# Kernel optimization log

Hardware: AMD Instinct MI355X
Metric: run time of the kernel (lower is better)

Reference implementation:

```python
import jax, jax.numpy as jnp
import numpy as np

R = 12          # resolution (H = W = G); L = R**3 = 1728
HEADS = 12


def setup_inputs() -> dict:
    key = jax.random.key(0)
    k1, k2, k3 = jax.random.split(key, 3)
    B, L, C = 4, R ** 3, 768
    qkv = jax.random.normal(k1, (3, B, L, C), dtype=jnp.float32)
    lepe_w = jax.random.normal(k2, (C, 1, 3, 3, 3), dtype=jnp.float32) * 0.05
    lepe_b = jax.random.normal(k3, (C,), dtype=jnp.float32) * 0.01
    return {"qkv": qkv, "lepe_w": lepe_w, "lepe_b": lepe_b}


def reference(qkv, lepe_w, lepe_b):
    # qkv: [3, B, L, C]; idx=0 => window == full volume, so attention is dense over L.
    q, k, v = qkv[0], qkv[1], qkv[2]
    B, L, C = q.shape
    hd = C // HEADS
    scale = hd ** -0.5

    # im2cswin with full-volume window preserves token order: [B, L, C] -> [B, H, L, d]
    qh = q.reshape(B, L, HEADS, hd).transpose(0, 2, 1, 3)
    kh = k.reshape(B, L, HEADS, hd).transpose(0, 2, 1, 3)

    # get_lepe: v -> [B, C, R, R, R], depthwise 3x3x3 conv (groups=C)
    v_img = v.transpose(0, 2, 1).reshape(B, C, R, R, R)
    lepe = jax.lax.conv_general_dilated(
        v_img, lepe_w, window_strides=(1, 1, 1), padding="SAME",
        dimension_numbers=("NCDHW", "OIDHW", "NCDHW"), feature_group_count=C,
    ) + lepe_b[None, :, None, None, None]
    lepe = lepe.reshape(B, HEADS, hd, L).transpose(0, 1, 3, 2)   # [B, H, L, d]
    vh = v_img.reshape(B, HEADS, hd, L).transpose(0, 1, 3, 2)    # [B, H, L, d]

    attn = jax.nn.softmax(jnp.einsum("bhqd,bhkd->bhqk", qh * scale, kh), axis=-1)
    out = jnp.einsum("bhqk,bhkd->bhqd", attn, vh) + lepe          # [B, H, L, d]

    # windows2img with full window is an inverse reshape back to [B, L, C]
    return out.transpose(0, 2, 1, 3).reshape(B, L, C)
```

## Files before the change

kernel.cpp:

```cpp
#include <hip/hip_runtime.h>

#define RR 12
#define LL 1728
#define CC 768
#define HEADS 12
#define HD 64
#define BATCH 4

typedef __attribute__((ext_vector_type(8))) short bf8;
typedef __attribute__((ext_vector_type(4))) float f4;

__device__ inline unsigned short f2bf(float x) {
  unsigned int u = __float_as_uint(x);
  return (unsigned short)((u + 0x7FFFu + ((u >> 16) & 1u)) >> 16);
}
__device__ inline unsigned short f2bfr(float x) {
  return (unsigned short)((__float_as_uint(x) + 0x8000u) >> 16);
}

__device__ inline float fast_exp2(float x) {
#if __has_builtin(__builtin_amdgcn_exp2f)
  return __builtin_amdgcn_exp2f(x);
#else
  return exp2f(x);
#endif
}

__device__ inline void gld16(const unsigned short* g, unsigned short* l) {
  __builtin_amdgcn_global_load_lds((const __attribute__((address_space(1))) unsigned int*)g,
                                   (__attribute__((address_space(3))) unsigned int*)l, 16, 0, 0);
}

#define QSCALE 0.1803368801111244f

#define NLEPE 5184
#define NPREP 1296

__global__ __launch_bounds__(256) void combined_kernel(const float* __restrict__ qkv,
                                                       const float* __restrict__ w,
                                                       const float* __restrict__ bias,
                                                       unsigned short* __restrict__ qb,
                                                       unsigned short* __restrict__ kb,
                                                       unsigned short* __restrict__ vT,
                                                       float* __restrict__ out) {
  __shared__ __align__(16) unsigned char smem[27648];
  const int bid = blockIdx.x;
  const int t = threadIdx.x;

  if (bid < NLEPE) {
    const int xg = (bid % 3) * 4;
    const int line = (bid / 3) % 144;
    const int ct = (bid / 432) % 3;
    const int b = bid / 1296;
    const int z = line / RR;
    const int y = line % RR;
    const int c0 = ct * 256;
    const int c = c0 + t;
    float* w_lds = (float*)smem;

    {
      const float* wsrc = w + (size_t)c0 * 27;
#pragma unroll
      for (int i = 0; i < 7; ++i) {
        const int idx = i * 256 + t;
        if (idx < 1728) *(float4*)&w_lds[idx * 4] = *(const float4*)&wsrc[idx * 4];
      }
    }
    __syncthreads();
    float wreg[27];
#pragma unroll
    for (int j = 0; j < 27; ++j) wreg[j] = w_lds[t * 27 + j];

    const float* vb = qkv + ((size_t)(2 * BATCH + b)) * LL * CC + c;
    const float bv = bias[c];
    float acc[4] = {bv, bv, bv, bv};

#pragma unroll
    for (int dz = -1; dz <= 1; ++dz) {
#pragma unroll
      for (int dy = -1; dy <= 1; ++dy) {
        const int zz = z + dz, yy = y + dy;
        const bool lineok = ((unsigned)zz < RR) & ((unsigned)yy < RR);
        const int base = (zz * RR + yy) * RR;
        float v6[6];
#pragma unroll
        for (int p = 0; p < 6; ++p) {
          const int xx = xg - 1 + p;
          const bool ok = lineok & ((unsigned)xx < RR);
          const int lp = ok ? base + xx : 0;
          const float vv = vb[(size_t)lp * CC];
          v6[p] = ok ? vv : 0.f;
        }
        const int jb = ((dz + 1) * 3 + (dy + 1)) * 3;
        const float wL = wreg[jb], wC = wreg[jb + 1], wR = wreg[jb + 2];
#pragma unroll
        for (int i = 0; i < 4; ++i)
          acc[i] += wL * v6[i] + wC * v6[i + 1] + wR * v6[i + 2];
      }
    }
    const size_t obase = ((size_t)b * LL + line * RR + xg) * CC + c;
#pragma unroll
    for (int i = 0; i < 4; ++i) out[obase + (size_t)i * CC] = acc[i];

  } else {
    const int p = bid - NLEPE;
    const int lt = p % 27;
    const int h = (p / 27) % HEADS;
    const int b = p / (27 * HEADS);
    unsigned short* tl = (unsigned short*)smem;

    {
      const int r0 = t >> 4;
      const int c4 = (t & 15) * 4;
#pragma unroll
      for (int pi = 0; pi < 4; ++pi) {
        const int row = lt * 64 + pi * 16 + r0;
        const size_t off = ((size_t)b * LL + row) * CC + h * HD + c4;
        const float4 qv = *(const float4*)(qkv + off);
        ushort4 oq;
        oq.x = f2bf(qv.x * QSCALE); oq.y = f2bf(qv.y * QSCALE);
        oq.z = f2bf(qv.z * QSCALE); oq.w = f2bf(qv.w * QSCALE);
        *(ushort4*)(qb + off) = oq;
        const float4 kv = *(const float4*)(qkv + (size_t)BATCH * LL * CC + off);
        ushort4 ok;
        ok.x = f2bf(kv.x); ok.y = f2bf(kv.y); ok.z = f2bf(kv.z); ok.w = f2bf(kv.w);
        *(ushort4*)(kb + off) = ok;
      }
    }

    const float* vsrc = qkv + ((size_t)(2 * BATCH + b)) * LL * CC;
#pragma unroll
    for (int it = 0; it < 4; ++it) {
      const int idx = it * 256 + t;
      const int lrow = idx >> 4;
      const int c4 = (idx & 15) * 4;
      const float4 vv = *(const float4*)(vsrc + (size_t)(lt * 64 + lrow) * CC + h * HD + c4);
      tl[(c4 + 0) * 65 + lrow] = f2bf(vv.x);
      tl[(c4 + 1) * 65 + lrow] = f2bf(vv.y);
      tl[(c4 + 2) * 65 + lrow] = f2bf(vv.z);
      tl[(c4 + 3) * 65 + lrow] = f2bf(vv.w);
    }
    __syncthreads();
#pragma unroll
    for (int it = 0; it < 4; ++it) {
      const int idx = it * 256 + t;
      const int drow = idx >> 4;
      const int s4 = (idx & 15) * 4;
      const int lb = s4 >> 2;
      ushort4 o;
      o.x = tl[drow * 65 + lb];
      o.y = tl[drow * 65 + 16 + lb];
      o.z = tl[drow * 65 + 32 + lb];
      o.w = tl[drow * 65 + 48 + lb];
      *(ushort4*)(vT + (((size_t)(b * HEADS + h) * HD + drow) * LL) + lt * 64 + s4) = o;
    }
  }
}

__global__ __launch_bounds__(256) void attn_kernel(const unsigned short* __restrict__ qb,
                                                   const unsigned short* __restrict__ kb,
                                                   const unsigned short* __restrict__ vT,
                                                   float* __restrict__ out) {
  __shared__ unsigned short k_lds[2][64 * 64];
  __shared__ unsigned short v_lds[2][64 * 64];
  __shared__ unsigned short p_lds[4][16 * 72];

  const int qt = blockIdx.x;
  const int h = blockIdx.y;
  const int b = blockIdx.z;
  const int t = threadIdx.x;
  const int lane = t & 63;
  const int wave = t >> 6;
  const int m = lane & 15;
  const int quad = lane >> 4;

  bf8 qf[2];
  {
    const size_t qbase = ((size_t)(b * LL + qt * 64 + wave * 16 + m)) * CC + h * HD;
    qf[0] = *(const bf8*)(qb + qbase + quad * 8);
    qf[1] = *(const bf8*)(qb + qbase + 32 + quad * 8);
  }

  int koff[2], voff[2], ldsb[2];
#pragma unroll
  for (int j = 0; j < 2; ++j) {
    const int cidx = (j * 4 + wave) * 64 + lane;
    const int row = cidx >> 3;
    const int sc = (cidx & 7) ^ (row & 7);
    koff[j] = row * CC + sc * 8;
    voff[j] = row * LL + sc * 8;
    ldsb[j] = (j * 4 + wave) * 512;
  }

  const unsigned short* kgb = kb + (size_t)b * LL * CC + h * HD;
  const unsigned short* vgb = vT + ((size_t)(b * HEADS + h) * HD) * LL;

  gld16(kgb + koff[0], &k_lds[0][ldsb[0]]);
  gld16(kgb + koff[1], &k_lds[0][ldsb[1]]);
  gld16(vgb + voff[0], &v_lds[0][ldsb[0]]);
  gld16(vgb + voff[1], &v_lds[0][ldsb[1]]);

  f4 o_acc[4] = {};
  float psum[4] = {0.f, 0.f, 0.f, 0.f};

#define ATTN_BODY(KT, CUR)                                                              \
  {                                                                                     \
    __syncthreads();            \
    if ((KT) < 26) {                                                                    \
      const size_t ko = (size_t)((KT) + 1) * 64 * CC;                                   \
      const int vo = ((KT) + 1) * 64;                                                   \
      gld16(kgb + ko + koff[0], &k_lds[(CUR) ^ 1][ldsb[0]]);                            \
      gld16(kgb + ko + koff[1], &k_lds[(CUR) ^ 1][ldsb[1]]);                            \
      gld16(vgb + vo + voff[0], &v_lds[(CUR) ^ 1][ldsb[0]]);                            \
      gld16(vgb + vo + voff[1], &v_lds[(CUR) ^ 1][ldsb[1]]);                            \
    }                                                                                   \
    f4 s_acc[4] = {};                                                                   \
    _Pragma("unroll")                                                                   \
    for (int nt = 0; nt < 4; ++nt) {                                                    \
      _Pragma("unroll")                                                                 \
      for (int ks = 0; ks < 2; ++ks) {                                                  \
        const int cc = ((ks * 4 + quad) ^ (m & 7)) * 8;                                 \
        const bf8 kf = *(const bf8*)&k_lds[CUR][(nt * 16 + m) * 64 + cc];               \
        s_acc[nt] = __builtin_amdgcn_mfma_f32_16x16x32_bf16(qf[ks], kf, s_acc[nt], 0, 0, 0); \
      }                                                                                 \
    }                                                                                   \
    _Pragma("unroll")                                                                   \
    for (int r = 0; r < 4; ++r) {                                                       \
      const float p0 = fast_exp2(s_acc[0][r]);                                          \
      const float p1 = fast_exp2(s_acc[1][r]);                                          \
      const float p2 = fast_exp2(s_acc[2][r]);                                          \
      const float p3 = fast_exp2(s_acc[3][r]);                                          \
      psum[r] += (p0 + p1) + (p2 + p3);                                                 \
      ushort4 pk;        \
      pk.x = f2bfr(p0); pk.y = f2bfr(p1); pk.z = f2bfr(p2); pk.w = f2bfr(p3);           \
      *(ushort4*)&p_lds[wave][(quad * 4 + r) * 72 + m * 4] = pk;                        \
    }                                                                                   \
    __asm__ volatile("s_waitcnt lgkmcnt(0)" ::: "memory");      \
    bf8 pf[2];                                                                          \
    _Pragma("unroll")                                                                   \
    for (int ks = 0; ks < 2; ++ks)                                                      \
      pf[ks] = *(const bf8*)&p_lds[wave][m * 72 + ks * 32 + quad * 8];                  \
    _Pragma("unroll")                                                                   \
    for (int nt = 0; nt < 4; ++nt) {                                                    \
      _Pragma("unroll")                                                                 \
      for (int ks = 0; ks < 2; ++ks) {                                                  \
        const int cc = ((ks * 4 + quad) ^ (m & 7)) * 8;                                 \
        const bf8 vf = *(const bf8*)&v_lds[CUR][(nt * 16 + m) * 64 + cc];               \
        o_acc[nt] = __builtin_amdgcn_mfma_f32_16x16x32_bf16(pf[ks], vf, o_acc[nt], 0, 0, 0); \
      }                                                                                 \
    }                                                                                   \
  }

  for (int ktp = 0; ktp < 13; ++ktp) {
    const int kt0 = ktp * 2;
    ATTN_BODY(kt0, 0)
    ATTN_BODY(kt0 + 1, 1)
  }
  ATTN_BODY(26, 0)
#undef ATTN_BODY

#pragma unroll
  for (int r = 0; r < 4; ++r) {
    float s = psum[r];
    s += __shfl_xor(s, 1);
    s += __shfl_xor(s, 2);
    s += __shfl_xor(s, 4);
    s += __shfl_xor(s, 8);
    const float inv = 1.0f / s;
    const int row = qt * 64 + wave * 16 + quad * 4 + r;
    float* op = out + ((size_t)b * LL + row) * CC + h * HD;
#pragma unroll
    for (int nt = 0; nt < 4; ++nt) {
      const int cix = nt * 16 + m;
      op[cix] = op[cix] + o_acc[nt][r] * inv;
    }
  }
}

extern "C" void kernel_launch(void* const* d_in, const int* in_sizes, int n_in,
                              void* d_out, int out_size, void* d_ws, size_t ws_size,
                              hipStream_t stream) {
  (void)in_sizes; (void)n_in; (void)ws_size; (void)out_size;
  const float* qkv = (const float*)d_in[0];
  const float* lepe_w = (const float*)d_in[1];
  const float* lepe_b = (const float*)d_in[2];
  float* out = (float*)d_out;

  const size_t NE = (size_t)BATCH * LL * CC;
  unsigned short* qb = (unsigned short*)d_ws;
  unsigned short* kb = qb + NE;
  unsigned short* vT = kb + NE;

  combined_kernel<<<dim3(NLEPE + NPREP), 256, 0, stream>>>(qkv, lepe_w, lepe_b, qb, kb, vT, out);
  attn_kernel<<<dim3(27, HEADS, BATCH), 256, 0, stream>>>(qb, kb, vT, out);
}
```

Before: 194.1 us.

## Keep softmax probabilities in registers via transposed MFMA and permuted V layout

Swaps the MFMA operand order so the score tile comes out transposed, letting each lane pack its exp2 probabilities directly into the B-operand fragment for the PV product instead of staging them through per-wave LDS. The V transpose prep kernel permutes the key order within each 64-key tile to match this register fragment layout. The row-sum reduction shrinks to two cross-quad shuffles, and the epilogue does float4 read-modify-writes to the output. This removes LDS writes, reads and a waitcnt per key tile, at the cost of coupling the V workspace layout to the MFMA lane mapping.

```diff
diff --git a/kernel.cpp b/kernel.cpp
--- a/kernel.cpp
+++ b/kernel.cpp
@@ -145,13 +145,14 @@
     for (int it = 0; it < 4; ++it) {
       const int idx = it * 256 + t;
       const int drow = idx >> 4;
-      const int s4 = (idx & 15) * 4;
-      const int lb = s4 >> 2;
+      const int u = idx & 15;
+      const int s4 = u * 4;
+      const int kbase = (((u >> 3) * 2 + (u & 1)) << 4) + (((u >> 1) & 3) << 2);
       ushort4 o;
-      o.x = tl[drow * 65 + lb];
-      o.y = tl[drow * 65 + 16 + lb];
-      o.z = tl[drow * 65 + 32 + lb];
-      o.w = tl[drow * 65 + 48 + lb];
+      o.x = tl[drow * 65 + kbase + 0];
+      o.y = tl[drow * 65 + kbase + 1];
+      o.z = tl[drow * 65 + kbase + 2];
+      o.w = tl[drow * 65 + kbase + 3];
       *(ushort4*)(vT + (((size_t)(b * HEADS + h) * HD + drow) * LL) + lt * 64 + s4) = o;
     }
   }
@@ -163,7 +164,6 @@
                                                    float* __restrict__ out) {
   __shared__ unsigned short k_lds[2][64 * 64];
   __shared__ unsigned short v_lds[2][64 * 64];
-  __shared__ unsigned short p_lds[4][16 * 72];
 
   const int qt = blockIdx.x;
   const int h = blockIdx.y;
@@ -201,7 +201,7 @@
   gld16(vgb + voff[1], &v_lds[0][ldsb[1]]);
 
   f4 o_acc[4] = {};
-  float psum[4] = {0.f, 0.f, 0.f, 0.f};
+  float psum = 0.f;
 
 #define ATTN_BODY(KT, CUR)                                                              \
   {                                                                                     \
@@ -221,32 +221,33 @@
       for (int ks = 0; ks < 2; ++ks) {                                                  \
         const int cc = ((ks * 4 + quad) ^ (m & 7)) * 8;                                 \
         const bf8 kf = *(const bf8*)&k_lds[CUR][(nt * 16 + m) * 64 + cc];               \
-        s_acc[nt] = __builtin_amdgcn_mfma_f32_16x16x32_bf16(qf[ks], kf, s_acc[nt], 0, 0, 0); \
+        s_acc[nt] = __builtin_amdgcn_mfma_f32_16x16x32_bf16(kf, qf[ks], s_acc[nt], 0, 0, 0); \
       }                                                                                 \
     }                                                                                   \
-    _Pragma("unroll")                                                                   \
-    for (int r = 0; r < 4; ++r) {                                                       \
-      const float p0 = fast_exp2(s_acc[0][r]);                                          \
-      const float p1 = fast_exp2(s_acc[1][r]);                                          \
-      const float p2 = fast_exp2(s_acc[2][r]);                                          \
-      const float p3 = fast_exp2(s_acc[3][r]);                                          \
-      psum[r] += (p0 + p1) + (p2 + p3);                                                 \
-      ushort4 pk;        \
-      pk.x = f2bfr(p0); pk.y = f2bfr(p1); pk.z = f2bfr(p2); pk.w = f2bfr(p3);           \
-      *(ushort4*)&p_lds[wave][(quad * 4 + r) * 72 + m * 4] = pk;                        \
-    }                                                                                   \
-    __asm__ volatile("s_waitcnt lgkmcnt(0)" ::: "memory");      \
     bf8 pf[2];                                                                          \
     _Pragma("unroll")                                                                   \
-    for (int ks = 0; ks < 2; ++ks)                                                      \
-      pf[ks] = *(const bf8*)&p_lds[wave][m * 72 + ks * 32 + quad * 8];                  \
+    for (int ks = 0; ks < 2; ++ks) {                                                    \
+      union { bf8 v; unsigned int w[4]; } pu;                                           \
+      _Pragma("unroll")                                                                 \
+      for (int bb = 0; bb < 2; ++bb) {                                                  \
+        const int nt = ks * 2 + bb;                                                     \
+        const float p0 = fast_exp2(s_acc[nt][0]);                                       \
+        const float p1 = fast_exp2(s_acc[nt][1]);                                       \
+        const float p2 = fast_exp2(s_acc[nt][2]);                                       \
+        const float p3 = fast_exp2(s_acc[nt][3]);                                       \
+        psum += (p0 + p1) + (p2 + p3);                                                  \
+        pu.w[bb * 2 + 0] = (unsigned int)f2bfr(p0) | ((unsigned int)f2bfr(p1) << 16);   \
+        pu.w[bb * 2 + 1] = (unsigned int)f2bfr(p2) | ((unsigned int)f2bfr(p3) << 16);   \
+      }                                                                                 \
+      pf[ks] = pu.v;                                                                    \
+    }                                                                                   \
     _Pragma("unroll")                                                                   \
     for (int nt = 0; nt < 4; ++nt) {                                                    \
       _Pragma("unroll")                                                                 \
       for (int ks = 0; ks < 2; ++ks) {                                                  \
         const int cc = ((ks * 4 + quad) ^ (m & 7)) * 8;                                 \
         const bf8 vf = *(const bf8*)&v_lds[CUR][(nt * 16 + m) * 64 + cc];               \
-        o_acc[nt] = __builtin_amdgcn_mfma_f32_16x16x32_bf16(pf[ks], vf, o_acc[nt], 0, 0, 0); \
+        o_acc[nt] = __builtin_amdgcn_mfma_f32_16x16x32_bf16(vf, pf[ks], o_acc[nt], 0, 0, 0); \
       }                                                                                 \
     }                                                                                   \
   }
@@ -259,21 +260,20 @@
   ATTN_BODY(26, 0)
 #undef ATTN_BODY
 
-#pragma unroll
-  for (int r = 0; r < 4; ++r) {
-    float s = psum[r];
-    s += __shfl_xor(s, 1);
-    s += __shfl_xor(s, 2);
-    s += __shfl_xor(s, 4);
-    s += __shfl_xor(s, 8);
-    const float inv = 1.0f / s;
-    const int row = qt * 64 + wave * 16 + quad * 4 + r;
-    float* op = out + ((size_t)b * LL + row) * CC + h * HD;
-#pragma unroll
-    for (int nt = 0; nt < 4; ++nt) {
-      const int cix = nt * 16 + m;
-      op[cix] = op[cix] + o_acc[nt][r] * inv;
-    }
+  float s = psum;
+  s += __shfl_xor(s, 16);
+  s += __shfl_xor(s, 32);
+  const float inv = 1.0f / s;
+  const int rowq = qt * 64 + wave * 16 + m;
+  float* op = out + ((size_t)b * LL + rowq) * CC + h * HD + quad * 4;
+#pragma unroll
+  for (int nt = 0; nt < 4; ++nt) {
+    float4 o4 = *(float4*)&op[nt * 16];
+    o4.x += o_acc[nt][0] * inv;
+    o4.y += o_acc[nt][1] * inv;
+    o4.z += o_acc[nt][2] * inv;
+    o4.w += o_acc[nt][3] * inv;
+    *(float4*)&op[nt * 16] = o4;
   }
 }
 
```

Result: no change. 193.1 us (-0.5%).
